# Kernel tuning notes

Measured on AMD Instinct MI355X. Metric: run time of the kernel, lower is better.

The kernel has to match this reference:

```python
import jax, jax.numpy as jnp
import numpy as np

DIM = 192
HID = 128
EPS = 1e-8
ITERS = 3
LN_EPS = 1e-5
SCALE = DIM ** (-0.5)


def layer_norm(x, w, b):
    mu = x.mean(axis=-1, keepdims=True)
    var = ((x - mu) ** 2).mean(axis=-1, keepdims=True)
    return (x - mu) * jax.lax.rsqrt(var + LN_EPS) * w + b


def gru_cell(x, h, Wih, Whh, bih, bhh):
    # PyTorch GRUCell: gates ordered (r, z, n)
    gx = x @ Wih.T + bih          # [M, 3*DIM]
    gh = h @ Whh.T + bhh          # [M, 3*DIM]
    xr, xz, xn = jnp.split(gx, 3, axis=-1)
    hr, hz, hn = jnp.split(gh, 3, axis=-1)
    r = jax.nn.sigmoid(xr + hr)
    z = jax.nn.sigmoid(xz + hz)
    n = jnp.tanh(xn + r * hn)
    return (1.0 - z) * n + z * h


def setup_inputs() -> dict:
    key = jax.random.key(0)
    ks = jax.random.split(key, 12)
    B, N, K = 64, 4096, 11
    s = 0.02
    return {
        "inputs": jax.random.normal(ks[0], (B, N, DIM), jnp.float32),
        "noise": jax.random.normal(ks[1], (B, K, DIM), jnp.float32),
        "slots_mu": jax.random.normal(ks[2], (1, 1, DIM), jnp.float32),
        "slots_sigma": jax.random.uniform(ks[3], (1, 1, DIM), jnp.float32),
        "ln_in_w": jnp.ones((DIM,), jnp.float32),
        "ln_in_b": jnp.zeros((DIM,), jnp.float32),
        "ln_slots_w": jnp.ones((DIM,), jnp.float32),
        "ln_slots_b": jnp.zeros((DIM,), jnp.float32),
        "ln_mlp_w": jnp.ones((DIM,), jnp.float32),
        "ln_mlp_b": jnp.zeros((DIM,), jnp.float32),
        "Wq": jax.random.normal(ks[4], (DIM, DIM), jnp.float32) * s,
        "bq": jnp.zeros((DIM,), jnp.float32),
        "Wk": jax.random.normal(ks[5], (DIM, DIM), jnp.float32) * s,
        "bk": jnp.zeros((DIM,), jnp.float32),
        "Wv": jax.random.normal(ks[6], (DIM, DIM), jnp.float32) * s,
        "bv": jnp.zeros((DIM,), jnp.float32),
        "gru_Wih": jax.random.normal(ks[7], (3 * DIM, DIM), jnp.float32) * s,
        "gru_Whh": jax.random.normal(ks[8], (3 * DIM, DIM), jnp.float32) * s,
        "gru_bih": jnp.zeros((3 * DIM,), jnp.float32),
        "gru_bhh": jnp.zeros((3 * DIM,), jnp.float32),
        "mlp_W1": jax.random.normal(ks[9], (DIM, HID), jnp.float32) * s,
        "mlp_b1": jnp.zeros((HID,), jnp.float32),
        "mlp_W2": jax.random.normal(ks[10], (HID, DIM), jnp.float32) * s,
        "mlp_b2": jnp.zeros((DIM,), jnp.float32),
        "n_slots": 11,
    }


def reference(inputs, noise, slots_mu, slots_sigma,
              ln_in_w, ln_in_b, ln_slots_w, ln_slots_b, ln_mlp_w, ln_mlp_b,
              Wq, bq, Wk, bk, Wv, bv,
              gru_Wih, gru_Whh, gru_bih, gru_bhh,
              mlp_W1, mlp_b1, mlp_W2, mlp_b2, n_slots):
    B, N, _ = inputs.shape
    # slots ~ Normal(mu, sigma), reparameterized with fixed noise
    slots = slots_mu + slots_sigma * noise            # [B, K, D]
    x = layer_norm(inputs, ln_in_w, ln_in_b)
    key_vec = x @ Wk + bk                             # [B, N, D]
    val_vec = x @ Wv + bv                             # [B, N, D]
    attn_output = None
    for _ in range(ITERS):
        slots_prev = slots
        s_n = layer_norm(slots, ln_slots_w, ln_slots_b)
        q = s_n @ Wq + bq                             # [B, K, D]
        dots = jnp.einsum('bkd,bnd->bkn', q, key_vec) * SCALE
        attn = jax.nn.softmax(dots, axis=1) + EPS     # softmax over slots axis
        attn_output = attn
        attn = attn / attn.sum(axis=-1, keepdims=True)
        updates = jnp.einsum('bnd,bkn->bkd', val_vec, attn)
        h = gru_cell(updates.reshape(-1, DIM), slots_prev.reshape(-1, DIM),
                     gru_Wih, gru_Whh, gru_bih, gru_bhh)
        slots = h.reshape(B, -1, DIM)
        m = layer_norm(slots, ln_mlp_w, ln_mlp_b)
        m = jax.nn.relu(m @ mlp_W1 + mlp_b1) @ mlp_W2 + mlp_b2
        slots = slots + m
    return (slots, attn_output)
```

## Files before the change

### kernel.cpp

```cpp
#include <hip/hip_runtime.h>
#include <hip/hip_bf16.h>
#include <cstdint>
#include <cstddef>

#define DIM 192
#define NSL 11
#define NB 64
#define NN 4096
#define HIDN 128
#define NCHP 16
#define TROWS 32
#define NT 8
#define LN_EPS 1e-5f
#define EPS_A 1e-8f
#define SCALE_Q 0.07216878364870323f

__device__ __forceinline__ float wred(float v) {
#pragma unroll
  for (int m = 32; m; m >>= 1) v += __shfl_xor(v, m, 64);
  return v;
}

typedef const __attribute__((address_space(1))) void gas_void;
typedef __attribute__((address_space(3))) void las_void;
__device__ __forceinline__ void gload_lds16(const void* g, void* l) {
  __builtin_amdgcn_global_load_lds((gas_void*)g, (las_void*)l, 16, 0, 0);
}

__global__ __launch_bounds__(256) void k_tr(
    const float* __restrict__ Wih, const float* __restrict__ Whh, const float* __restrict__ Wk,
    float* __restrict__ WihT, float* __restrict__ WhhT, float* __restrict__ WkT) {
  __shared__ float t[64][65];
  int tile = blockIdx.x;
  const float* src; float* dst; int R, C;
  if (tile < 27)      { src = Wih; dst = WihT; R = 576; C = 192; }
  else if (tile < 54) { src = Whh; dst = WhhT; R = 576; C = 192; tile -= 27; }
  else                { src = Wk;  dst = WkT;  R = 192; C = 192; tile -= 54; }
  const int ntc = C >> 6;
  const int tr = tile / ntc, tc = tile % ntc;
  const int lane = threadIdx.x & 63, w = threadIdx.x >> 6;
#pragma unroll
  for (int i = 0; i < 16; ++i) {
    int row = w * 16 + i;
    t[row][lane] = src[(size_t)(tr * 64 + row) * C + tc * 64 + lane];
  }
  __syncthreads();
#pragma unroll
  for (int i = 0; i < 16; ++i) {
    int row = w * 16 + i;
    dst[(size_t)(tc * 64 + row) * R + tr * 64 + lane] = t[lane][row];
  }
}

__global__ __launch_bounds__(192) void k_prep(
    const float* __restrict__ lnw, const float* __restrict__ lnb,
    const float* __restrict__ Wq, const float* __restrict__ bq,
    const float* __restrict__ WkT, const float* __restrict__ bk,
    const float* __restrict__ xw, const float* __restrict__ xb,
    const float* __restrict__ noise, const float* __restrict__ mu0, const float* __restrict__ sig,
    float* __restrict__ slots_ws,
    float* __restrict__ qt, float* __restrict__ t0g, float* __restrict__ cpg) {
  const int b = blockIdx.x, kg = blockIdx.y, tid = threadIdx.x;
  const int k0 = kg * 3, kcnt = (kg == 3) ? 2 : 3;
  const int wave = tid >> 6, lane = tid & 63;
  const int j = tid;
  __shared__ __align__(16) float sn[3][DIM];
  __shared__ __align__(16) float qb[3][DIM];
  __shared__ float red[3][3][2];

#pragma unroll
  for (int kk = 0; kk < 3; ++kk) {
    if (kk < kcnt) {
      float v = mu0[j] + sig[j] * noise[(size_t)(b * NSL + k0 + kk) * DIM + j];
      sn[kk][j] = v;
      slots_ws[(size_t)(b * NSL + k0 + kk) * DIM + j] = v;
    } else sn[kk][j] = 0.f;
  }
  __syncthreads();

  for (int kk = wave; kk < 3; kk += 3) {
    float a = sn[kk][lane], c = sn[kk][lane + 64], e = sn[kk][lane + 128];
    float s = wred(a + c + e), ss = wred(a * a + c * c + e * e);
    float mu = s * (1.0f / DIM), var = ss * (1.0f / DIM) - mu * mu;
    float rstd = rsqrtf(var + LN_EPS);
    sn[kk][lane]       = (a - mu) * rstd * lnw[lane]       + lnb[lane];
    sn[kk][lane + 64]  = (c - mu) * rstd * lnw[lane + 64]  + lnb[lane + 64];
    sn[kk][lane + 128] = (e - mu) * rstd * lnw[lane + 128] + lnb[lane + 128];
  }
  __syncthreads();

  float acc[3];
  const float bj = bq[j];
#pragma unroll
  for (int kk = 0; kk < 3; ++kk) acc[kk] = bj;
  for (int d = 0; d < DIM; d += 4) {
    float w0 = Wq[(d + 0) * DIM + j], w1 = Wq[(d + 1) * DIM + j];
    float w2 = Wq[(d + 2) * DIM + j], w3 = Wq[(d + 3) * DIM + j];
#pragma unroll
    for (int kk = 0; kk < 3; ++kk) {
      float4 s4 = *(const float4*)&sn[kk][d];
      acc[kk] = fmaf(s4.w, w3, fmaf(s4.z, w2, fmaf(s4.y, w1, fmaf(s4.x, w0, acc[kk]))));
    }
  }
#pragma unroll
  for (int kk = 0; kk < 3; ++kk) qb[kk][j] = acc[kk];
  __syncthreads();

  float qk[3];
#pragma unroll
  for (int kk = 0; kk < 3; ++kk) qk[kk] = 0.f;
  for (int d = 0; d < DIM; d += 4) {
    float w0 = WkT[(d + 0) * DIM + j], w1 = WkT[(d + 1) * DIM + j];
    float w2 = WkT[(d + 2) * DIM + j], w3 = WkT[(d + 3) * DIM + j];
#pragma unroll
    for (int kk = 0; kk < 3; ++kk) {
      float4 q4 = *(const float4*)&qb[kk][d];
      qk[kk] = fmaf(q4.w, w3, fmaf(q4.z, w2, fmaf(q4.y, w1, fmaf(q4.x, w0, qk[kk]))));
    }
  }
  const float wj = xw[j], bxj = xb[j], bkj = bk[j];
#pragma unroll
  for (int kk = 0; kk < 3; ++kk) {
    float qtv = SCALE_Q * wj * qk[kk];
    if (kk < kcnt) qt[(size_t)(b * NSL + k0 + kk) * DIM + j] = qtv;
    float r1 = wred(qtv);
    float r2 = wred(SCALE_Q * (bxj * qk[kk] + qb[kk][j] * bkj));
    if (lane == 0) { red[wave][kk][0] = r1; red[wave][kk][1] = r2; }
  }
  __syncthreads();
  if (tid < kcnt) {
    t0g[b * NSL + k0 + tid] = red[0][tid][0] + red[1][tid][0] + red[2][tid][0];
    cpg[b * NSL + k0 + tid] = red[0][tid][1] + red[1][tid][1] + red[2][tid][1];
  }
}

__global__ __launch_bounds__(256) void k_iter(
    const float* __restrict__ x, const float* __restrict__ qt,
    const float* __restrict__ t0g, const float* __restrict__ cpg,
    float* __restrict__ attn_out, float* __restrict__ P1p,
    float* __restrict__ S_p, float* __restrict__ m1_p) {
  __shared__ __align__(16) float xs[2][TROWS * DIM];
  __shared__ __align__(16) float qs[NSL * DIM];
  __shared__ __align__(16) float a_lds[TROWS][12];
  __shared__ float rs_lds[TROWS];
  __shared__ float t0s[NSL], cps[NSL];
  __shared__ float redS[4][NSL], redM[4][NSL];

  const int b = blockIdx.x, ch = blockIdx.y, tid = threadIdx.x;
  const int lane = tid & 63, wv = tid >> 6;
  const int widx = tid & 15, g = tid >> 4;

  const float* xbase = x + ((size_t)b * NN + ch * 256) * DIM;

  {
#pragma unroll
    for (int i = 0; i < 6; ++i) {
      int c = i * 4 + wv;
      gload_lds16(xbase + c * 256 + lane * 4, &xs[0][c * 256]);
    }
  }
  {
    const float4* src = (const float4*)(qt + (size_t)b * NSL * DIM);
    float4* dst = (float4*)qs;
    dst[tid] = src[tid];
    dst[256 + tid] = src[256 + tid];
    if (tid < 16) dst[512 + tid] = src[512 + tid];
  }
  if (tid < NSL) { t0s[tid] = t0g[b * NSL + tid]; cps[tid] = cpg[b * NSL + tid]; }

  float acc[3][NSL], sS[NSL], sM[NSL];
#pragma unroll
  for (int k = 0; k < NSL; ++k) {
    acc[0][k] = 0.f; acc[1][k] = 0.f; acc[2][k] = 0.f;
    sS[k] = 0.f; sM[k] = 0.f;
  }

#pragma unroll 1
  for (int T = 0; T < NT; ++T) {
    const int cur = T & 1;
    __syncthreads();
    if (T < NT - 1) {
      const float* src = xbase + (size_t)(T + 1) * TROWS * DIM;
      float* dstb = &xs[cur ^ 1][0];
#pragma unroll
      for (int i = 0; i < 6; ++i) {
        int c = i * 4 + wv;
        gload_lds16(src + c * 256 + lane * 4, dstb + c * 256);
      }
      asm volatile("s_waitcnt vmcnt(6)" ::: "memory");
    } else {
      asm volatile("s_waitcnt vmcnt(0)" ::: "memory");
    }
    __builtin_amdgcn_s_barrier();
    const float* xc = &xs[cur][0];

    float dot[2][NSL], st_s[2], st_ss[2];
#pragma unroll
    for (int rr = 0; rr < 2; ++rr) {
      st_s[rr] = 0.f; st_ss[rr] = 0.f;
#pragma unroll
      for (int k = 0; k < NSL; ++k) dot[rr][k] = 0.f;
    }
#pragma unroll
    for (int w = 0; w < 3; ++w) {
      const int c4 = widx + 16 * w;
      float4 xr[2];
#pragma unroll
      for (int rr = 0; rr < 2; ++rr) {
        xr[rr] = ((const float4*)xc)[(2 * g + rr) * 48 + c4];
        st_s[rr] += (xr[rr].x + xr[rr].y) + (xr[rr].z + xr[rr].w);
        st_ss[rr] = fmaf(xr[rr].x, xr[rr].x, fmaf(xr[rr].y, xr[rr].y,
                    fmaf(xr[rr].z, xr[rr].z, fmaf(xr[rr].w, xr[rr].w, st_ss[rr]))));
      }
#pragma unroll
      for (int k = 0; k < NSL; ++k) {
        float4 qv = *(const float4*)&qs[k * DIM + 4 * c4];
#pragma unroll
        for (int rr = 0; rr < 2; ++rr)
          dot[rr][k] = fmaf(xr[rr].w, qv.w, fmaf(xr[rr].z, qv.z,
                       fmaf(xr[rr].y, qv.y, fmaf(xr[rr].x, qv.x, dot[rr][k]))));
      }
    }
#pragma unroll
    for (int m = 1; m <= 8; m <<= 1) {
#pragma unroll
      for (int rr = 0; rr < 2; ++rr) {
        st_s[rr] += __shfl_xor(st_s[rr], m, 64);
        st_ss[rr] += __shfl_xor(st_ss[rr], m, 64);
#pragma unroll
        for (int k = 0; k < NSL; ++k) dot[rr][k] += __shfl_xor(dot[rr][k], m, 64);
      }
    }
    if ((widx & 7) == 0) {
      const int hi = widx >> 3;
      const int r = 2 * g + hi;
      float dsel[NSL];
#pragma unroll
      for (int k = 0; k < NSL; ++k) dsel[k] = (widx == 0) ? dot[0][k] : dot[1][k];
      float sts  = (widx == 0) ? st_s[0]  : st_s[1];
      float stss = (widx == 0) ? st_ss[0] : st_ss[1];
      float mu = sts * (1.0f / DIM);
      float var = stss * (1.0f / DIM) - mu * mu;
      float rstd = rsqrtf(var + LN_EPS);
      float murstd = mu * rstd;
      float dv[NSL];
#pragma unroll
      for (int k = 0; k < NSL; ++k) dv[k] = fmaf(rstd, dsel[k], fmaf(-murstd, t0s[k], cps[k]));
      float mx = dv[0];
#pragma unroll
      for (int k = 1; k < NSL; ++k) mx = fmaxf(mx, dv[k]);
      float es[NSL], sum = 0.f;
#pragma unroll
      for (int k = 0; k < NSL; ++k) { es[k] = __expf(dv[k] - mx); sum += es[k]; }
      float inv = 1.0f / sum;
#pragma unroll
      for (int k = 0; k < NSL; ++k) {
        float a = fmaf(es[k], inv, EPS_A);
        a_lds[r][k] = a;
        sS[k] += a;
        sM[k] = fmaf(a, murstd, sM[k]);
      }
      rs_lds[r] = rstd;
    }
    asm volatile("s_waitcnt lgkmcnt(0)" ::: "memory");
    __builtin_amdgcn_s_barrier();

    {
      int idx = tid;
      attn_out[((size_t)(b * NSL + (idx >> 5))) * NN + ch * 256 + T * TROWS + (idx & 31)]
          = a_lds[idx & 31][idx >> 5];
      idx = tid + 256;
      if (idx < NSL * TROWS)
        attn_out[((size_t)(b * NSL + (idx >> 5))) * NN + ch * 256 + T * TROWS + (idx & 31)]
            = a_lds[idx & 31][idx >> 5];
    }
#pragma unroll 4
    for (int i = 0; i < 8; ++i) {
      const int r = 4 * i + wv;
      float rst = rs_lds[r];
      float4 a0 = *(const float4*)&a_lds[r][0];
      float4 a1 = *(const float4*)&a_lds[r][4];
      float4 a2 = *(const float4*)&a_lds[r][8];
#pragma unroll
      for (int j = 0; j < 3; ++j) {
        const int col = lane + 64 * j;
        float t1 = rst * xc[r * DIM + col];
        acc[j][0]  = fmaf(a0.x, t1, acc[j][0]);
        acc[j][1]  = fmaf(a0.y, t1, acc[j][1]);
        acc[j][2]  = fmaf(a0.z, t1, acc[j][2]);
        acc[j][3]  = fmaf(a0.w, t1, acc[j][3]);
        acc[j][4]  = fmaf(a1.x, t1, acc[j][4]);
        acc[j][5]  = fmaf(a1.y, t1, acc[j][5]);
        acc[j][6]  = fmaf(a1.z, t1, acc[j][6]);
        acc[j][7]  = fmaf(a1.w, t1, acc[j][7]);
        acc[j][8]  = fmaf(a2.x, t1, acc[j][8]);
        acc[j][9]  = fmaf(a2.y, t1, acc[j][9]);
        acc[j][10] = fmaf(a2.z, t1, acc[j][10]);
      }
    }
  }

  __syncthreads();
  float* accbuf = &xs[0][0];
#pragma unroll
  for (int j = 0; j < 3; ++j)
#pragma unroll
    for (int k = 0; k < NSL; ++k)
      accbuf[tid * 33 + j * 11 + k] = acc[j][k];
  __syncthreads();
  if (tid < DIM) {
    const int l = tid & 63, j = tid >> 6;
#pragma unroll
    for (int k = 0; k < NSL; ++k) {
      float v = accbuf[(l) * 33 + j * 11 + k] + accbuf[(64 + l) * 33 + j * 11 + k]
              + accbuf[(128 + l) * 33 + j * 11 + k] + accbuf[(192 + l) * 33 + j * 11 + k];
      P1p[(((size_t)b * NCHP + ch) * NSL + k) * DIM + tid] = v;
    }
  }
#pragma unroll
  for (int k = 0; k < NSL; ++k) { sS[k] = wred(sS[k]); sM[k] = wred(sM[k]); }
  if (lane == 0) {
#pragma unroll
    for (int k = 0; k < NSL; ++k) { redS[wv][k] = sS[k]; redM[wv][k] = sM[k]; }
  }
  __syncthreads();
  if (tid < NSL) {
    S_p[((size_t)b * NCHP + ch) * NSL + tid]  = redS[0][tid] + redS[1][tid] + redS[2][tid] + redS[3][tid];
    m1_p[((size_t)b * NCHP + ch) * NSL + tid] = redM[0][tid] + redM[1][tid] + redM[2][tid] + redM[3][tid];
  }
}

__global__ __launch_bounds__(192) void k_step(
    const float* __restrict__ P1p, const float* __restrict__ m1_p, const float* __restrict__ S_p,
    const float* __restrict__ xw, const float* __restrict__ xb,
    const float* __restrict__ Wv, const float* __restrict__ bv,
    const float* __restrict__ slots_in,
    const float* __restrict__ WihT, const float* __restrict__ WhhT,
    const float* __restrict__ bih, const float* __restrict__ bhh,
    const float* __restrict__ mw, const float* __restrict__ mb,
    const float* __restrict__ W1, const float* __restrict__ b1,
    const float* __restrict__ W2, const float* __restrict__ b2,
    const float* __restrict__ sw, const float* __restrict__ sb,
    const float* __restrict__ Wq, const float* __restrict__ bq,
    const float* __restrict__ WkT, const float* __restrict__ bk,
    float* __restrict__ slots_ws, float* __restrict__ slots_out,
    float* __restrict__ qt, float* __restrict__ t0g, float* __restrict__ cpg) {
  const int b = blockIdx.x, kg = blockIdx.y, tid = threadIdx.x;
  const int k0 = kg * 3, kcnt = (kg == 3) ? 2 : 3;
  const int wave = tid >> 6, lane = tid & 63;
  const int j = tid;
  __shared__ __align__(16) float u[3][DIM];
  __shared__ __align__(16) float hp[3][DIM];
  __shared__ __align__(16) float h[3][DIM];
  __shared__ __align__(16) float hid[3][HIDN];
  __shared__ float red[3][3][2];

  const float wj = xw[j], bj = xb[j];
#pragma unroll
  for (int kk = 0; kk < 3; ++kk) {
    if (kk < kcnt) {
      float p = 0.f, S = 0.f, M = 0.f;
#pragma unroll
      for (int ch = 0; ch < NCHP; ++ch) {
        p += P1p[(((size_t)b * NCHP + ch) * NSL + k0 + kk) * DIM + j];
        S += S_p[((size_t)b * NCHP + ch) * NSL + k0 + kk];
        M += m1_p[((size_t)b * NCHP + ch) * NSL + k0 + kk];
      }
      float inv = 1.0f / S;
      u[kk][j]  = wj * (p - M) * inv + bj;
      hp[kk][j] = slots_in[(size_t)(b * NSL + k0 + kk) * DIM + j];
    } else { u[kk][j] = 0.f; hp[kk][j] = 0.f; }
  }
  __syncthreads();

  float upd[3];
  const float bvj = bv[j];
#pragma unroll
  for (int kk = 0; kk < 3; ++kk) upd[kk] = bvj;
  for (int d = 0; d < DIM; d += 4) {
    float w0 = Wv[(d + 0) * DIM + j], w1 = Wv[(d + 1) * DIM + j];
    float w2 = Wv[(d + 2) * DIM + j], w3 = Wv[(d + 3) * DIM + j];
#pragma unroll
    for (int kk = 0; kk < 3; ++kk) {
      float4 x4 = *(const float4*)&u[kk][d];
      upd[kk] = fmaf(x4.w, w3, fmaf(x4.z, w2, fmaf(x4.y, w1, fmaf(x4.x, w0, upd[kk]))));
    }
  }
  __syncthreads();
#pragma unroll
  for (int kk = 0; kk < 3; ++kk) u[kk][j] = upd[kk];
  __syncthreads();

  float xr[3], xz[3], xn[3], hr[3], hz[3], hn[3];
  {
    float br_ = bih[j], bz_ = bih[DIM + j], bn_ = bih[2 * DIM + j];
    float cr_ = bhh[j], cz_ = bhh[DIM + j], cn_ = bhh[2 * DIM + j];
#pragma unroll
    for (int kk = 0; kk < 3; ++kk) { xr[kk] = br_; xz[kk] = bz_; xn[kk] = bn_; hr[kk] = cr_; hz[kk] = cz_; hn[kk] = cn_; }
  }
  for (int d = 0; d < DIM; d += 2) {
#pragma unroll
    for (int dd = 0; dd < 2; ++dd) {
      const float* ihrow = WihT + (size_t)(d + dd) * 576;
      const float* hhrow = WhhT + (size_t)(d + dd) * 576;
      float ar = ihrow[j], az = ihrow[192 + j], an = ihrow[384 + j];
      float br = hhrow[j], bz = hhrow[192 + j], bn = hhrow[384 + j];
#pragma unroll
      for (int kk = 0; kk < 3; ++kk) {
        float uv = u[kk][d + dd];
        float pv = hp[kk][d + dd];
        xr[kk] = fmaf(uv, ar, xr[kk]);
        xz[kk] = fmaf(uv, az, xz[kk]);
        xn[kk] = fmaf(uv, an, xn[kk]);
        hr[kk] = fmaf(pv, br, hr[kk]);
        hz[kk] = fmaf(pv, bz, hz[kk]);
        hn[kk] = fmaf(pv, bn, hn[kk]);
      }
    }
  }
#pragma unroll
  for (int kk = 0; kk < 3; ++kk) {
    float r = 1.f / (1.f + __expf(-(xr[kk] + hr[kk])));
    float z = 1.f / (1.f + __expf(-(xz[kk] + hz[kk])));
    float n = tanhf(xn[kk] + r * hn[kk]);
    h[kk][j] = (1.f - z) * n + z * hp[kk][j];
  }
  __syncthreads();

  for (int kk = wave; kk < 3; kk += 3) {
    float a = h[kk][lane], c = h[kk][lane + 64], e = h[kk][lane + 128];
    float s = wred(a + c + e), ss = wred(a * a + c * c + e * e);
    float mu = s * (1.0f / DIM), var = ss * (1.0f / DIM) - mu * mu;
    float rstd = rsqrtf(var + LN_EPS);
    u[kk][lane]       = (a - mu) * rstd * mw[lane]       + mb[lane];
    u[kk][lane + 64]  = (c - mu) * rstd * mw[lane + 64]  + mb[lane + 64];
    u[kk][lane + 128] = (e - mu) * rstd * mw[lane + 128] + mb[lane + 128];
  }
  __syncthreads();

  for (int t = tid; t < kcnt * HIDN; t += 192) {
    int kk = t >> 7, c = t & (HIDN - 1);
    float acc = b1[c];
    for (int d = 0; d < DIM; d += 4) {
      float4 m4 = *(const float4*)&u[kk][d];
      acc = fmaf(m4.x, W1[(d + 0) * HIDN + c],
            fmaf(m4.y, W1[(d + 1) * HIDN + c],
            fmaf(m4.z, W1[(d + 2) * HIDN + c],
            fmaf(m4.w, W1[(d + 3) * HIDN + c], acc))));
    }
    hid[kk][c] = fmaxf(acc, 0.f);
  }
  __syncthreads();

#pragma unroll 1
  for (int kk = 0; kk < kcnt; ++kk) {
    float acc = b2[j];
    for (int c = 0; c < HIDN; c += 4) {
      float4 h4 = *(const float4*)&hid[kk][c];
      acc = fmaf(h4.x, W2[(c + 0) * DIM + j],
            fmaf(h4.y, W2[(c + 1) * DIM + j],
            fmaf(h4.z, W2[(c + 2) * DIM + j],
            fmaf(h4.w, W2[(c + 3) * DIM + j], acc))));
    }
    float outv = h[kk][j] + acc;
    size_t gi = (size_t)(b * NSL + k0 + kk) * DIM + j;
    slots_ws[gi] = outv;
    slots_out[gi] = outv;
    hp[kk][j] = outv;
  }
  __syncthreads();

  for (int kk = wave; kk < 3; kk += 3) {
    float a = hp[kk][lane], c = hp[kk][lane + 64], e = hp[kk][lane + 128];
    float s = wred(a + c + e), ss = wred(a * a + c * c + e * e);
    float mu = s * (1.0f / DIM), var = ss * (1.0f / DIM) - mu * mu;
    float rstd = rsqrtf(var + LN_EPS);
    u[kk][lane]       = (a - mu) * rstd * sw[lane]       + sb[lane];
    u[kk][lane + 64]  = (c - mu) * rstd * sw[lane + 64]  + sb[lane + 64];
    u[kk][lane + 128] = (e - mu) * rstd * sw[lane + 128] + sb[lane + 128];
  }
  __syncthreads();

  float qacc[3];
  const float bqj = bq[j];
#pragma unroll
  for (int kk = 0; kk < 3; ++kk) qacc[kk] = bqj;
  for (int d = 0; d < DIM; d += 4) {
    float w0 = Wq[(d + 0) * DIM + j], w1 = Wq[(d + 1) * DIM + j];
    float w2 = Wq[(d + 2) * DIM + j], w3 = Wq[(d + 3) * DIM + j];
#pragma unroll
    for (int kk = 0; kk < 3; ++kk) {
      float4 s4 = *(const float4*)&u[kk][d];
      qacc[kk] = fmaf(s4.w, w3, fmaf(s4.z, w2, fmaf(s4.y, w1, fmaf(s4.x, w0, qacc[kk]))));
    }
  }
  __syncthreads();
#pragma unroll
  for (int kk = 0; kk < 3; ++kk) h[kk][j] = qacc[kk];
  __syncthreads();

  float qk[3];
#pragma unroll
  for (int kk = 0; kk < 3; ++kk) qk[kk] = 0.f;
  for (int d = 0; d < DIM; d += 4) {
    float w0 = WkT[(d + 0) * DIM + j], w1 = WkT[(d + 1) * DIM + j];
    float w2 = WkT[(d + 2) * DIM + j], w3 = WkT[(d + 3) * DIM + j];
#pragma unroll
    for (int kk = 0; kk < 3; ++kk) {
      float4 q4 = *(const float4*)&h[kk][d];
      qk[kk] = fmaf(q4.w, w3, fmaf(q4.z, w2, fmaf(q4.y, w1, fmaf(q4.x, w0, qk[kk]))));
    }
  }
  const float wxj = xw[j], bxj = xb[j], bkj = bk[j];
#pragma unroll
  for (int kk = 0; kk < 3; ++kk) {
    float qtv = SCALE_Q * wxj * qk[kk];
    if (kk < kcnt) qt[(size_t)(b * NSL + k0 + kk) * DIM + j] = qtv;
    float r1 = wred(qtv);
    float r2 = wred(SCALE_Q * (bxj * qk[kk] + h[kk][j] * bkj));
    if (lane == 0) { red[wave][kk][0] = r1; red[wave][kk][1] = r2; }
  }
  __syncthreads();
  if (tid < kcnt) {
    t0g[b * NSL + k0 + tid] = red[0][tid][0] + red[1][tid][0] + red[2][tid][0];
    cpg[b * NSL + k0 + tid] = red[0][tid][1] + red[1][tid][1] + red[2][tid][1];
  }
}

extern "C" void kernel_launch(void* const* d_in, const int* in_sizes, int n_in,
                              void* d_out, int out_size, void* d_ws, size_t ws_size,
                              hipStream_t stream) {
  const float* inputs      = (const float*)d_in[0];
  const float* noise       = (const float*)d_in[1];
  const float* slots_mu    = (const float*)d_in[2];
  const float* slots_sigma = (const float*)d_in[3];
  const float* ln_in_w     = (const float*)d_in[4];
  const float* ln_in_b     = (const float*)d_in[5];
  const float* ln_slots_w  = (const float*)d_in[6];
  const float* ln_slots_b  = (const float*)d_in[7];
  const float* ln_mlp_w    = (const float*)d_in[8];
  const float* ln_mlp_b    = (const float*)d_in[9];
  const float* Wq  = (const float*)d_in[10];
  const float* bq  = (const float*)d_in[11];
  const float* Wk  = (const float*)d_in[12];
  const float* bk  = (const float*)d_in[13];
  const float* Wv  = (const float*)d_in[14];
  const float* bv  = (const float*)d_in[15];
  const float* Wih = (const float*)d_in[16];
  const float* Whh = (const float*)d_in[17];
  const float* bih = (const float*)d_in[18];
  const float* bhh = (const float*)d_in[19];
  const float* W1  = (const float*)d_in[20];
  const float* b1  = (const float*)d_in[21];
  const float* W2  = (const float*)d_in[22];
  const float* b2  = (const float*)d_in[23];

  float* out = (float*)d_out;
  float* slots_out = out;
  float* attn_out  = out + NB * NSL * DIM;

  char* w = (char*)d_ws;
  float* slots = (float*)w;
  float* qt    = (float*)(w + 540672);
  float* t0g   = (float*)(w + 1081344);
  float* cpg   = (float*)(w + 1084160);
  float* P1p   = (float*)(w + 1086976);
  float* S_p   = (float*)(w + 9737728);
  float* m1_p  = (float*)(w + 9782784);
  float* WihT  = (float*)(w + 9827840);
  float* WhhT  = (float*)(w + 10270208);
  float* WkT   = (float*)(w + 10712576);

  k_tr<<<63, 256, 0, stream>>>(Wih, Whh, Wk, WihT, WhhT, WkT);
  k_prep<<<dim3(NB, 4), 192, 0, stream>>>(ln_slots_w, ln_slots_b, Wq, bq, WkT, bk,
                                          ln_in_w, ln_in_b, noise, slots_mu, slots_sigma,
                                          slots, qt, t0g, cpg);
  for (int it = 0; it < 3; ++it) {
    k_iter<<<dim3(NB, NCHP), 256, 0, stream>>>(inputs, qt, t0g, cpg, attn_out, P1p, S_p, m1_p);
    k_step<<<dim3(NB, 4), 192, 0, stream>>>(P1p, m1_p, S_p, ln_in_w, ln_in_b, Wv, bv, slots,
                                            WihT, WhhT, bih, bhh, ln_mlp_w, ln_mlp_b,
                                            W1, b1, W2, b2, ln_slots_w, ln_slots_b,
                                            Wq, bq, WkT, bk, slots, slots_out, qt, t0g, cpg);
  }
}
```

Baseline: 771.8 us.

## Split k_step reductions across 768 threads; single-buffer k_iter LDS for occupancy

k_step now launches 768 threads per block and splits every matrix-vector product (Wv, GRU, MLP, Wq, Wk) along the input dimension into four partial sums combined through shared memory. This shortens each thread's serial dependency chain in the latency-bound small-batch slot update. k_iter drops its double-buffered LDS tile in favour of a single buffer, requests 4 waves per EU, and reduces its accumulator-combine scratch space, all to raise occupancy. The cost in k_iter is that global-to-LDS loads are no longer overlapped with compute, and k_step gains extra barriers and shared-memory traffic.

```diff
diff --git a/kernel.cpp b/kernel.cpp
--- a/kernel.cpp
+++ b/kernel.cpp
@@ -134,12 +134,12 @@
   }
 }
 
-__global__ __launch_bounds__(256) void k_iter(
+__global__ __launch_bounds__(256) __attribute__((amdgpu_waves_per_eu(4, 4))) void k_iter(
     const float* __restrict__ x, const float* __restrict__ qt,
     const float* __restrict__ t0g, const float* __restrict__ cpg,
     float* __restrict__ attn_out, float* __restrict__ P1p,
     float* __restrict__ S_p, float* __restrict__ m1_p) {
-  __shared__ __align__(16) float xs[2][TROWS * DIM];
+  __shared__ __align__(16) float xs[TROWS * DIM];
   __shared__ __align__(16) float qs[NSL * DIM];
   __shared__ __align__(16) float a_lds[TROWS][12];
   __shared__ float rs_lds[TROWS];
@@ -152,12 +152,10 @@
 
   const float* xbase = x + ((size_t)b * NN + ch * 256) * DIM;
 
-  {
-#pragma unroll
-    for (int i = 0; i < 6; ++i) {
-      int c = i * 4 + wv;
-      gload_lds16(xbase + c * 256 + lane * 4, &xs[0][c * 256]);
-    }
+#pragma unroll
+  for (int i = 0; i < 6; ++i) {
+    int c = i * 4 + wv;
+    gload_lds16(xbase + c * 256 + lane * 4, &xs[c * 256]);
   }
   {
     const float4* src = (const float4*)(qt + (size_t)b * NSL * DIM);
@@ -177,22 +175,19 @@
 
 #pragma unroll 1
   for (int T = 0; T < NT; ++T) {
-    const int cur = T & 1;
-    __syncthreads();
-    if (T < NT - 1) {
-      const float* src = xbase + (size_t)(T + 1) * TROWS * DIM;
-      float* dstb = &xs[cur ^ 1][0];
+    if (T == 0) {
+      __syncthreads();
+    } else {
+      __syncthreads();
+      const float* src = xbase + (size_t)T * TROWS * DIM;
 #pragma unroll
       for (int i = 0; i < 6; ++i) {
         int c = i * 4 + wv;
-        gload_lds16(src + c * 256 + lane * 4, dstb + c * 256);
+        gload_lds16(src + c * 256 + lane * 4, &xs[c * 256]);
       }
-      asm volatile("s_waitcnt vmcnt(6)" ::: "memory");
-    } else {
       asm volatile("s_waitcnt vmcnt(0)" ::: "memory");
-    }
-    __builtin_amdgcn_s_barrier();
-    const float* xc = &xs[cur][0];
+      __builtin_amdgcn_s_barrier();
+    }
 
     float dot[2][NSL], st_s[2], st_ss[2];
 #pragma unroll
@@ -207,7 +202,7 @@
       float4 xr[2];
 #pragma unroll
       for (int rr = 0; rr < 2; ++rr) {
-        xr[rr] = ((const float4*)xc)[(2 * g + rr) * 48 + c4];
+        xr[rr] = ((const float4*)xs)[(2 * g + rr) * 48 + c4];
         st_s[rr] += (xr[rr].x + xr[rr].y) + (xr[rr].z + xr[rr].w);
         st_ss[rr] = fmaf(xr[rr].x, xr[rr].x, fmaf(xr[rr].y, xr[rr].y,
                     fmaf(xr[rr].z, xr[rr].z, fmaf(xr[rr].w, xr[rr].w, st_ss[rr]))));
@@ -284,7 +279,7 @@
 #pragma unroll
       for (int j = 0; j < 3; ++j) {
         const int col = lane + 64 * j;
-        float t1 = rst * xc[r * DIM + col];
+        float t1 = rst * xs[r * DIM + col];
         acc[j][0]  = fmaf(a0.x, t1, acc[j][0]);
         acc[j][1]  = fmaf(a0.y, t1, acc[j][1]);
         acc[j][2]  = fmaf(a0.z, t1, acc[j][2]);
@@ -301,19 +296,29 @@
   }
 
   __syncthreads();
-  float* accbuf = &xs[0][0];
-#pragma unroll
-  for (int j = 0; j < 3; ++j)
-#pragma unroll
-    for (int k = 0; k < NSL; ++k)
-      accbuf[tid * 33 + j * 11 + k] = acc[j][k];
+  float* accbuf = &xs[0];
+  const int slot = tid & 127;
+  if (wv < 2) {
+#pragma unroll
+    for (int j = 0; j < 3; ++j)
+#pragma unroll
+      for (int k = 0; k < NSL; ++k)
+        accbuf[slot * 33 + j * 11 + k] = acc[j][k];
+  }
+  __syncthreads();
+  if (wv >= 2) {
+#pragma unroll
+    for (int j = 0; j < 3; ++j)
+#pragma unroll
+      for (int k = 0; k < NSL; ++k)
+        accbuf[slot * 33 + j * 11 + k] += acc[j][k];
+  }
   __syncthreads();
   if (tid < DIM) {
     const int l = tid & 63, j = tid >> 6;
 #pragma unroll
     for (int k = 0; k < NSL; ++k) {
-      float v = accbuf[(l) * 33 + j * 11 + k] + accbuf[(64 + l) * 33 + j * 11 + k]
-              + accbuf[(128 + l) * 33 + j * 11 + k] + accbuf[(192 + l) * 33 + j * 11 + k];
+      float v = accbuf[l * 33 + j * 11 + k] + accbuf[(64 + l) * 33 + j * 11 + k];
       P1p[(((size_t)b * NCHP + ch) * NSL + k) * DIM + tid] = v;
     }
   }
@@ -330,7 +335,8 @@
   }
 }
 
-__global__ __launch_bounds__(192) void k_step(
+#define TPBS 768
+__global__ __launch_bounds__(TPBS) void k_step(
     const float* __restrict__ P1p, const float* __restrict__ m1_p, const float* __restrict__ S_p,
     const float* __restrict__ xw, const float* __restrict__ xb,
     const float* __restrict__ Wv, const float* __restrict__ bv,
@@ -347,184 +353,250 @@
     float* __restrict__ qt, float* __restrict__ t0g, float* __restrict__ cpg) {
   const int b = blockIdx.x, kg = blockIdx.y, tid = threadIdx.x;
   const int k0 = kg * 3, kcnt = (kg == 3) ? 2 : 3;
-  const int wave = tid >> 6, lane = tid & 63;
-  const int j = tid;
+  const int q = tid / 192;
+  const int j = tid - q * 192;
+  const int lane = tid & 63;
+
+  __shared__ __align__(16) float red[4 * 18 * 192];
   __shared__ __align__(16) float u[3][DIM];
   __shared__ __align__(16) float hp[3][DIM];
   __shared__ __align__(16) float h[3][DIM];
   __shared__ __align__(16) float hid[3][HIDN];
-  __shared__ float red[3][3][2];
-
-  const float wj = xw[j], bj = xb[j];
+  __shared__ float sSp[3][16], sMp[3][16];
+  __shared__ float redw[3][3][2];
+
+#define RED(qq, gg, jj) red[(((qq) * 18 + (gg)) * 192) + (jj)]
+
+  int kidx[3];
+#pragma unroll
+  for (int kk = 0; kk < 3; ++kk) { int t = k0 + kk; kidx[kk] = t > NSL - 1 ? NSL - 1 : t; }
+
 #pragma unroll
   for (int kk = 0; kk < 3; ++kk) {
-    if (kk < kcnt) {
-      float p = 0.f, S = 0.f, M = 0.f;
-#pragma unroll
-      for (int ch = 0; ch < NCHP; ++ch) {
-        p += P1p[(((size_t)b * NCHP + ch) * NSL + k0 + kk) * DIM + j];
-        S += S_p[((size_t)b * NCHP + ch) * NSL + k0 + kk];
-        M += m1_p[((size_t)b * NCHP + ch) * NSL + k0 + kk];
-      }
-      float inv = 1.0f / S;
-      u[kk][j]  = wj * (p - M) * inv + bj;
-      hp[kk][j] = slots_in[(size_t)(b * NSL + k0 + kk) * DIM + j];
-    } else { u[kk][j] = 0.f; hp[kk][j] = 0.f; }
-  }
-  __syncthreads();
-
-  float upd[3];
-  const float bvj = bv[j];
-#pragma unroll
-  for (int kk = 0; kk < 3; ++kk) upd[kk] = bvj;
-  for (int d = 0; d < DIM; d += 4) {
-    float w0 = Wv[(d + 0) * DIM + j], w1 = Wv[(d + 1) * DIM + j];
-    float w2 = Wv[(d + 2) * DIM + j], w3 = Wv[(d + 3) * DIM + j];
-#pragma unroll
-    for (int kk = 0; kk < 3; ++kk) {
-      float4 x4 = *(const float4*)&u[kk][d];
-      upd[kk] = fmaf(x4.w, w3, fmaf(x4.z, w2, fmaf(x4.y, w1, fmaf(x4.x, w0, upd[kk]))));
-    }
-  }
-  __syncthreads();
-#pragma unroll
-  for (int kk = 0; kk < 3; ++kk) u[kk][j] = upd[kk];
-  __syncthreads();
-
-  float xr[3], xz[3], xn[3], hr[3], hz[3], hn[3];
-  {
-    float br_ = bih[j], bz_ = bih[DIM + j], bn_ = bih[2 * DIM + j];
-    float cr_ = bhh[j], cz_ = bhh[DIM + j], cn_ = bhh[2 * DIM + j];
-#pragma unroll
-    for (int kk = 0; kk < 3; ++kk) { xr[kk] = br_; xz[kk] = bz_; xn[kk] = bn_; hr[kk] = cr_; hz[kk] = cz_; hn[kk] = cn_; }
-  }
-  for (int d = 0; d < DIM; d += 2) {
-#pragma unroll
-    for (int dd = 0; dd < 2; ++dd) {
-      const float* ihrow = WihT + (size_t)(d + dd) * 576;
-      const float* hhrow = WhhT + (size_t)(d + dd) * 576;
+    float p = 0.f;
+#pragma unroll
+    for (int c = 0; c < 4; ++c) {
+      int ch = q * 4 + c;
+      p += P1p[(((size_t)b * NCHP + ch) * NSL + kidx[kk]) * DIM + j];
+    }
+    RED(q, kk, j) = p;
+  }
+  if (tid < 48) {
+    int kk = tid >> 4, ch = tid & 15;
+    sSp[kk][ch] = S_p[((size_t)b * NCHP + ch) * NSL + kidx[kk]];
+    sMp[kk][ch] = m1_p[((size_t)b * NCHP + ch) * NSL + kidx[kk]];
+  }
+  if (q == 0) {
+#pragma unroll
+    for (int kk = 0; kk < 3; ++kk)
+      hp[kk][j] = slots_in[(size_t)(b * NSL + kidx[kk]) * DIM + j];
+  }
+  __syncthreads();
+  if (tid < 576) {
+    const int kk = q;
+    float p = RED(0, kk, j) + RED(1, kk, j) + RED(2, kk, j) + RED(3, kk, j);
+    float S = 0.f, M = 0.f;
+#pragma unroll
+    for (int ch = 0; ch < 16; ++ch) { S += sSp[kk][ch]; M += sMp[kk][ch]; }
+    u[kk][j] = xw[j] * (p - M) / S + xb[j];
+  }
+  __syncthreads();
+
+  {
+    float p0 = 0.f, p1 = 0.f, p2 = 0.f;
+    const int d0 = q * 48;
+#pragma unroll 4
+    for (int d = d0; d < d0 + 48; ++d) {
+      float w = Wv[d * DIM + j];
+      p0 = fmaf(u[0][d], w, p0);
+      p1 = fmaf(u[1][d], w, p1);
+      p2 = fmaf(u[2][d], w, p2);
+    }
+    RED(q, 0, j) = p0; RED(q, 1, j) = p1; RED(q, 2, j) = p2;
+  }
+  __syncthreads();
+  if (tid < 576) {
+    const int kk = q;
+    u[kk][j] = bv[j] + RED(0, kk, j) + RED(1, kk, j) + RED(2, kk, j) + RED(3, kk, j);
+  }
+  __syncthreads();
+
+  {
+    float pxr[3] = {0,0,0}, pxz[3] = {0,0,0}, pxn[3] = {0,0,0};
+    float phr[3] = {0,0,0}, phz[3] = {0,0,0}, phn[3] = {0,0,0};
+    const int d0 = q * 48;
+#pragma unroll 2
+    for (int d = d0; d < d0 + 48; ++d) {
+      const float* ihrow = WihT + (size_t)d * 576;
+      const float* hhrow = WhhT + (size_t)d * 576;
       float ar = ihrow[j], az = ihrow[192 + j], an = ihrow[384 + j];
       float br = hhrow[j], bz = hhrow[192 + j], bn = hhrow[384 + j];
 #pragma unroll
       for (int kk = 0; kk < 3; ++kk) {
-        float uv = u[kk][d + dd];
-        float pv = hp[kk][d + dd];
-        xr[kk] = fmaf(uv, ar, xr[kk]);
-        xz[kk] = fmaf(uv, az, xz[kk]);
-        xn[kk] = fmaf(uv, an, xn[kk]);
-        hr[kk] = fmaf(pv, br, hr[kk]);
-        hz[kk] = fmaf(pv, bz, hz[kk]);
-        hn[kk] = fmaf(pv, bn, hn[kk]);
+        float uv = u[kk][d], pv = hp[kk][d];
+        pxr[kk] = fmaf(uv, ar, pxr[kk]);
+        pxz[kk] = fmaf(uv, az, pxz[kk]);
+        pxn[kk] = fmaf(uv, an, pxn[kk]);
+        phr[kk] = fmaf(pv, br, phr[kk]);
+        phz[kk] = fmaf(pv, bz, phz[kk]);
+        phn[kk] = fmaf(pv, bn, phn[kk]);
       }
     }
-  }
-#pragma unroll
-  for (int kk = 0; kk < 3; ++kk) {
-    float r = 1.f / (1.f + __expf(-(xr[kk] + hr[kk])));
-    float z = 1.f / (1.f + __expf(-(xz[kk] + hz[kk])));
-    float n = tanhf(xn[kk] + r * hn[kk]);
+#pragma unroll
+    for (int kk = 0; kk < 3; ++kk) {
+      RED(q, 0 + kk, j)  = pxr[kk];  RED(q, 3 + kk, j)  = pxz[kk];
+      RED(q, 6 + kk, j)  = pxn[kk];  RED(q, 9 + kk, j)  = phr[kk];
+      RED(q, 12 + kk, j) = phz[kk];  RED(q, 15 + kk, j) = phn[kk];
+    }
+  }
+  __syncthreads();
+  if (tid < 576) {
+    const int kk = q;
+    float xr = bih[j]       + RED(0,0+kk,j)  + RED(1,0+kk,j)  + RED(2,0+kk,j)  + RED(3,0+kk,j);
+    float xz = bih[192 + j] + RED(0,3+kk,j)  + RED(1,3+kk,j)  + RED(2,3+kk,j)  + RED(3,3+kk,j);
+    float xn = bih[384 + j] + RED(0,6+kk,j)  + RED(1,6+kk,j)  + RED(2,6+kk,j)  + RED(3,6+kk,j);
+    float hr = bhh[j]       + RED(0,9+kk,j)  + RED(1,9+kk,j)  + RED(2,9+kk,j)  + RED(3,9+kk,j);
+    float hz = bhh[192 + j] + RED(0,12+kk,j) + RED(1,12+kk,j) + RED(2,12+kk,j) + RED(3,12+kk,j);
+    float hn = bhh[384 + j] + RED(0,15+kk,j) + RED(1,15+kk,j) + RED(2,15+kk,j) + RED(3,15+kk,j);
+    float r = 1.f / (1.f + __expf(-(xr + hr)));
+    float z = 1.f / (1.f + __expf(-(xz + hz)));
+    float n = tanhf(xn + r * hn);
     h[kk][j] = (1.f - z) * n + z * hp[kk][j];
   }
   __syncthreads();
 
-  for (int kk = wave; kk < 3; kk += 3) {
-    float a = h[kk][lane], c = h[kk][lane + 64], e = h[kk][lane + 128];
-    float s = wred(a + c + e), ss = wred(a * a + c * c + e * e);
-    float mu = s * (1.0f / DIM), var = ss * (1.0f / DIM) - mu * mu;
-    float rstd = rsqrtf(var + LN_EPS);
-    u[kk][lane]       = (a - mu) * rstd * mw[lane]       + mb[lane];
-    u[kk][lane + 64]  = (c - mu) * rstd * mw[lane + 64]  + mb[lane + 64];
-    u[kk][lane + 128] = (e - mu) * rstd * mw[lane + 128] + mb[lane + 128];
-  }
-  __syncthreads();
-
-  for (int t = tid; t < kcnt * HIDN; t += 192) {
-    int kk = t >> 7, c = t & (HIDN - 1);
-    float acc = b1[c];
-    for (int d = 0; d < DIM; d += 4) {
-      float4 m4 = *(const float4*)&u[kk][d];
-      acc = fmaf(m4.x, W1[(d + 0) * HIDN + c],
-            fmaf(m4.y, W1[(d + 1) * HIDN + c],
-            fmaf(m4.z, W1[(d + 2) * HIDN + c],
-            fmaf(m4.w, W1[(d + 3) * HIDN + c], acc))));
-    }
-    hid[kk][c] = fmaxf(acc, 0.f);
-  }
-  __syncthreads();
-
-#pragma unroll 1
-  for (int kk = 0; kk < kcnt; ++kk) {
-    float acc = b2[j];
-    for (int c = 0; c < HIDN; c += 4) {
-      float4 h4 = *(const float4*)&hid[kk][c];
-      acc = fmaf(h4.x, W2[(c + 0) * DIM + j],
-            fmaf(h4.y, W2[(c + 1) * DIM + j],
-            fmaf(h4.z, W2[(c + 2) * DIM + j],
-            fmaf(h4.w, W2[(c + 3) * DIM + j], acc))));
-    }
-    float outv = h[kk][j] + acc;
-    size_t gi = (size_t)(b * NSL + k0 + kk) * DIM + j;
-    slots_ws[gi] = outv;
-    slots_out[gi] = outv;
+  {
+    const int wv = tid >> 6;
+    if (wv < 3) {
+      const int kk = wv;
+      float a = h[kk][lane], c = h[kk][lane + 64], e = h[kk][lane + 128];
+      float s = wred(a + c + e), ss = wred(a * a + c * c + e * e);
+      float mu = s * (1.0f / DIM), var = ss * (1.0f / DIM) - mu * mu;
+      float rstd = rsqrtf(var + LN_EPS);
+      u[kk][lane]       = (a - mu) * rstd * mw[lane]       + mb[lane];
+      u[kk][lane + 64]  = (c - mu) * rstd * mw[lane + 64]  + mb[lane + 64];
+      u[kk][lane + 128] = (e - mu) * rstd * mw[lane + 128] + mb[lane + 128];
+    }
+  }
+  __syncthreads();
+
+  if (j < HIDN) {
+    float p0 = 0.f, p1 = 0.f, p2 = 0.f;
+    const int d0 = q * 48;
+#pragma unroll 4
+    for (int d = d0; d < d0 + 48; ++d) {
+      float w = W1[d * HIDN + j];
+      p0 = fmaf(u[0][d], w, p0);
+      p1 = fmaf(u[1][d], w, p1);
+      p2 = fmaf(u[2][d], w, p2);
+    }
+    RED(q, 0, j) = p0; RED(q, 1, j) = p1; RED(q, 2, j) = p2;
+  }
+  __syncthreads();
+  if (tid < 576 && j < HIDN) {
+    const int kk = q;
+    float v = b1[j] + RED(0, kk, j) + RED(1, kk, j) + RED(2, kk, j) + RED(3, kk, j);
+    hid[kk][j] = fmaxf(v, 0.f);
+  }
+  __syncthreads();
+
+  {
+    float p0 = 0.f, p1 = 0.f, p2 = 0.f;
+    const int c0 = q * 32;
+#pragma unroll 4
+    for (int c = c0; c < c0 + 32; ++c) {
+      float w = W2[c * DIM + j];
+      p0 = fmaf(hid[0][c], w, p0);
+      p1 = fmaf(hid[1][c], w, p1);
+      p2 = fmaf(hid[2][c], w, p2);
+    }
+    RED(q, 0, j) = p0; RED(q, 1, j) = p1; RED(q, 2, j) = p2;
+  }
+  __syncthreads();
+  if (tid < 576) {
+    const int kk = q;
+    float outv = h[kk][j] + b2[j] + RED(0, kk, j) + RED(1, kk, j) + RED(2, kk, j) + RED(3, kk, j);
+    if (kk < kcnt) {
+      size_t gi = (size_t)(b * NSL + k0 + kk) * DIM + j;
+      slots_ws[gi] = outv;
+      slots_out[gi] = outv;
+    }
     hp[kk][j] = outv;
   }
   __syncthreads();
 
-  for (int kk = wave; kk < 3; kk += 3) {
-    float a = hp[kk][lane], c = hp[kk][lane + 64], e = hp[kk][lane + 128];
-    float s = wred(a + c + e), ss = wred(a * a + c * c + e * e);
-    float mu = s * (1.0f / DIM), var = ss * (1.0f / DIM) - mu * mu;
-    float rstd = rsqrtf(var + LN_EPS);
-    u[kk][lane]       = (a - mu) * rstd * sw[lane]       + sb[lane];
-    u[kk][lane + 64]  = (c - mu) * rstd * sw[lane + 64]  + sb[lane + 64];
-    u[kk][lane + 128] = (e - mu) * rstd * sw[lane + 128] + sb[lane + 128];
-  }
-  __syncthreads();
-
-  float qacc[3];
-  const float bqj = bq[j];
-#pragma unroll
-  for (int kk = 0; kk < 3; ++kk) qacc[kk] = bqj;
-  for (int d = 0; d < DIM; d += 4) {
-    float w0 = Wq[(d + 0) * DIM + j], w1 = Wq[(d + 1) * DIM + j];
-    float w2 = Wq[(d + 2) * DIM + j], w3 = Wq[(d + 3) * DIM + j];
+  {
+    const int wv = tid >> 6;
+    if (wv < 3) {
+      const int kk = wv;
+      float a = hp[kk][lane], c = hp[kk][lane + 64], e = hp[kk][lane + 128];
+      float s = wred(a + c + e), ss = wred(a * a + c * c + e * e);
+      float mu = s * (1.0f / DIM), var = ss * (1.0f / DIM) - mu * mu;
+      float rstd = rsqrtf(var + LN_EPS);
+      u[kk][lane]       = (a - mu) * rstd * sw[lane]       + sb[lane];
+      u[kk][lane + 64]  = (c - mu) * rstd * sw[lane + 64]  + sb[lane + 64];
+      u[kk][lane + 128] = (e - mu) * rstd * sw[lane + 128] + sb[lane + 128];
+    }
+  }
+  __syncthreads();
+
+  {
+    float p0 = 0.f, p1 = 0.f, p2 = 0.f;
+    const int d0 = q * 48;
+#pragma unroll 4
+    for (int d = d0; d < d0 + 48; ++d) {
+      float w = Wq[d * DIM + j];
+      p0 = fmaf(u[0][d], w, p0);
+      p1 = fmaf(u[1][d], w, p1);
+      p2 = fmaf(u[2][d], w, p2);
+    }
+    RED(q, 0, j) = p0; RED(q, 1, j) = p1; RED(q, 2, j) = p2;
+  }
+  __syncthreads();
+  if (tid < 576) {
+    const int kk = q;
+    h[kk][j] = bq[j] + RED(0, kk, j) + RED(1, kk, j) + RED(2, kk, j) + RED(3, kk, j);
+  }
+  __syncthreads();
+
+  {
+    float p0 = 0.f, p1 = 0.f, p2 = 0.f;
+    const int d0 = q * 48;
+#pragma unroll 4
+    for (int d = d0; d < d0 + 48; ++d) {
+      float w = WkT[d * DIM + j];
+      p0 = fmaf(h[0][d], w, p0);
+      p1 = fmaf(h[1][d], w, p1);
+      p2 = fmaf(h[2][d], w, p2);
+    }
+    RED(q, 0, j) = p0; RED(q, 1, j) = p1; RED(q, 2, j) = p2;
+  }
+  __syncthreads();
+  if (tid < 576) {
+    const int kk = q;
+    u[kk][j] = RED(0, kk, j) + RED(1, kk, j) + RED(2, kk, j) + RED(3, kk, j);
+  }
+  __syncthreads();
+  if (tid < 192) {
+    const int wv = tid >> 6;
+    const float wxj = xw[j], bxj = xb[j], bkj = bk[j];
 #pragma unroll
     for (int kk = 0; kk < 3; ++kk) {
-      float4 s4 = *(const float4*)&u[kk][d];
-      qacc[kk] = fmaf(s4.w, w3, fmaf(s4.z, w2, fmaf(s4.y, w1, fmaf(s4.x, w0, qacc[kk]))));
-    }
-  }
-  __syncthreads();
-#pragma unroll
-  for (int kk = 0; kk < 3; ++kk) h[kk][j] = qacc[kk];
-  __syncthreads();
-
-  float qk[3];
-#pragma unroll
-  for (int kk = 0; kk < 3; ++kk) qk[kk] = 0.f;
-  for (int d = 0; d < DIM; d += 4) {
-    float w0 = WkT[(d + 0) * DIM + j], w1 = WkT[(d + 1) * DIM + j];
-    float w2 = WkT[(d + 2) * DIM + j], w3 = WkT[(d + 3) * DIM + j];
-#pragma unroll
-    for (int kk = 0; kk < 3; ++kk) {
-      float4 q4 = *(const float4*)&h[kk][d];
-      qk[kk] = fmaf(q4.w, w3, fmaf(q4.z, w2, fmaf(q4.y, w1, fmaf(q4.x, w0, qk[kk]))));
-    }
-  }
-  const float wxj = xw[j], bxj = xb[j], bkj = bk[j];
-#pragma unroll
-  for (int kk = 0; kk < 3; ++kk) {
-    float qtv = SCALE_Q * wxj * qk[kk];
-    if (kk < kcnt) qt[(size_t)(b * NSL + k0 + kk) * DIM + j] = qtv;
-    float r1 = wred(qtv);
-    float r2 = wred(SCALE_Q * (bxj * qk[kk] + h[kk][j] * bkj));
-    if (lane == 0) { red[wave][kk][0] = r1; red[wave][kk][1] = r2; }
+      float qk = u[kk][j];
+      float qv = h[kk][j];
+      float qtv = SCALE_Q * wxj * qk;
+      if (kk < kcnt) qt[(size_t)(b * NSL + k0 + kk) * DIM + j] = qtv;
+      float r1 = wred(qtv);
+      float r2 = wred(SCALE_Q * (bxj * qk + qv * bkj));
+      if (lane == 0) { redw[wv][kk][0] = r1; redw[wv][kk][1] = r2; }
+    }
   }
   __syncthreads();
   if (tid < kcnt) {
-    t0g[b * NSL + k0 + tid] = red[0][tid][0] + red[1][tid][0] + red[2][tid][0];
-    cpg[b * NSL + k0 + tid] = red[0][tid][1] + red[1][tid][1] + red[2][tid][1];
-  }
+    t0g[b * NSL + k0 + tid] = redw[0][tid][0] + redw[1][tid][0] + redw[2][tid][0];
+    cpg[b * NSL + k0 + tid] = redw[0][tid][1] + redw[1][tid][1] + redw[2][tid][1];
+  }
+#undef RED
 }
 
 extern "C" void kernel_launch(void* const* d_in, const int* in_sizes, int n_in,
@@ -577,9 +649,9 @@
                                           slots, qt, t0g, cpg);
   for (int it = 0; it < 3; ++it) {
     k_iter<<<dim3(NB, NCHP), 256, 0, stream>>>(inputs, qt, t0g, cpg, attn_out, P1p, S_p, m1_p);
-    k_step<<<dim3(NB, 4), 192, 0, stream>>>(P1p, m1_p, S_p, ln_in_w, ln_in_b, Wv, bv, slots,
-                                            WihT, WhhT, bih, bhh, ln_mlp_w, ln_mlp_b,
-                                            W1, b1, W2, b2, ln_slots_w, ln_slots_b,
-                                            Wq, bq, WkT, bk, slots, slots_out, qt, t0g, cpg);
+    k_step<<<dim3(NB, 4), TPBS, 0, stream>>>(P1p, m1_p, S_p, ln_in_w, ln_in_b, Wv, bv, slots,
+                                             WihT, WhhT, bih, bhh, ln_mlp_w, ln_mlp_b,
+                                             W1, b1, W2, b2, ln_slots_w, ln_slots_b,
+                                             Wq, bq, WkT, bk, slots, slots_out, qt, t0g, cpg);
   }
 }
```

Result: faster. 695.0 us (-9.9%).
